# Performance work log

Hardware: AMD Instinct MI355X
Metric: run time of the kernel (lower is better)

## Reference

```python
import jax, jax.numpy as jnp
import numpy as np
import math

D_MODEL = 512
PATCH_LENS = (8, 16, 32)
MAX_P = 32
TAU = 0.5


def _sinusoid_pe(num_pos, d_model):
    pos = jnp.arange(num_pos, dtype=jnp.float32)[:, None]
    div = jnp.exp(jnp.arange(0, d_model, 2, dtype=jnp.float32) * (-(math.log(10000.0) / d_model)))
    pe = jnp.zeros((num_pos, d_model), dtype=jnp.float32)
    pe = pe.at[:, 0::2].set(jnp.sin(pos * div))
    pe = pe.at[:, 1::2].set(jnp.cos(pos * div))
    return pe  # [num_pos, d_model]


def setup_inputs() -> dict:
    key = jax.random.key(0)
    ks = jax.random.split(key, 10)
    B, C, L = 32, 64, 512
    BC, R, n_exp = B * C, L // MAX_P, len(PATCH_LENS)
    x = jax.random.normal(ks[0], (B, C, L), dtype=jnp.float32)
    u = jax.random.uniform(ks[1], (BC, R, n_exp), dtype=jnp.float32, minval=1e-6, maxval=1.0 - 1e-6)
    gumbel = -jnp.log(-jnp.log(u))
    # router MLP: Linear(max_patch_len, 64) -> ReLU -> Linear(64, n_exp)
    s1 = 1.0 / math.sqrt(MAX_P)
    s2 = 1.0 / math.sqrt(64)
    cls_w1 = jax.random.uniform(ks[2], (MAX_P, 64), jnp.float32, -s1, s1)
    cls_b1 = jax.random.uniform(ks[3], (64,), jnp.float32, -s1, s1)
    cls_w2 = jax.random.uniform(ks[4], (64, n_exp), jnp.float32, -s2, s2)
    cls_b2 = jax.random.uniform(ks[5], (n_exp,), jnp.float32, -s2, s2)
    # per-patch-length expert embeddings: Linear(p, d_model, bias=False)
    emb_w8 = jax.random.uniform(ks[6], (8, D_MODEL), jnp.float32, -1 / math.sqrt(8), 1 / math.sqrt(8))
    emb_w16 = jax.random.uniform(ks[7], (16, D_MODEL), jnp.float32, -1 / math.sqrt(16), 1 / math.sqrt(16))
    emb_w32 = jax.random.uniform(ks[8], (32, D_MODEL), jnp.float32, -1 / math.sqrt(32), 1 / math.sqrt(32))
    return {"x": x, "gumbel": gumbel, "cls_w1": cls_w1, "cls_b1": cls_b1,
            "cls_w2": cls_w2, "cls_b2": cls_b2,
            "emb_w8": emb_w8, "emb_w16": emb_w16, "emb_w32": emb_w32}


def reference(x, gumbel, cls_w1, cls_b1, cls_w2, cls_b2, emb_w8, emb_w16, emb_w32):
    B, C, L = x.shape
    R = L // MAX_P                    # regions per series
    T = MAX_P // min(PATCH_LENS)      # target patches per region (mode='fixed')
    n_exp = len(PATCH_LENS)
    xr = x.reshape(B * C, R, MAX_P)   # [BC, R, P]

    # router MLP per region (vectorized over all regions)
    h = jax.nn.relu(jnp.einsum('brp,pk->brk', xr, cls_w1) + cls_b1)
    logits = jnp.einsum('brk,kn->brn', h, cls_w2) + cls_b2   # [BC, R, n_exp]

    # gumbel-softmax (tau=0.5, hard=True, straight-through)
    y_soft = jax.nn.softmax((logits + gumbel) / TAU, axis=-1)
    idx = jnp.argmax(y_soft, axis=-1)                         # [BC, R]
    y_hard = jax.nn.one_hot(idx, n_exp, dtype=y_soft.dtype)
    cls_soft = y_hard - jax.lax.stop_gradient(y_soft) + y_soft
    cls_pred = jnp.argmax(cls_soft, axis=-1)                  # [BC, R]

    # multi-branch expert embeddings, aligned to T patches via repeat_interleave+truncate
    expert_ws = (emb_w8, emb_w16, emb_w32)
    embs = []
    for p, w in zip(PATCH_LENS, expert_ws):
        n_p = MAX_P // p
        patches = xr.reshape(B * C, R, n_p, p)               # unfold(-1, p, p)
        rep = T - n_p + 1                                     # repeat_interleave factor
        sel = jnp.arange(T) // rep                            # truncated interleave indices
        patches = patches[:, :, sel, :]                       # [BC, R, T, p]
        embs.append(jnp.einsum('brtp,pd->brtd', patches, w))  # [BC, R, T, d]
    stack = jnp.stack(embs, axis=0)                           # [n_exp, BC, R, T, d]

    gates = jnp.transpose(cls_soft, (2, 0, 1))[..., None, None]  # [n_exp, BC, R, 1, 1]
    region_emb = (stack * gates).sum(axis=0)                  # [BC, R, T, d]

    x_patch = region_emb.reshape(B * C, R * T, D_MODEL)
    x_patch = x_patch + _sinusoid_pe(R * T, D_MODEL)[None]

    all_cls_pred = cls_pred.T.reshape(-1)                     # cat over regions along dim 0
    return x_patch, all_cls_pred
```

## Files before the change

### kernel.cpp

```cpp
#include <hip/hip_runtime.h>
#include <hip/hip_bf16.h>

#define BC 2048
#define RR 16
#define DM 512
#define NREG (BC * RR)
#define XPATCH ((size_t)BC * 64 * DM)

__global__ __launch_bounds__(256) void ape_fused(
    const float* __restrict__ x,
    const float* __restrict__ gumbel,
    const float* __restrict__ w1,
    const float* __restrict__ b1,
    const float* __restrict__ w2,
    const float* __restrict__ b2,
    const float* __restrict__ w8,
    const float* __restrict__ w16,
    const float* __restrict__ w32,
    float* __restrict__ out)
{
    const int rid = blockIdx.x;
    const int bc  = rid >> 4;
    const int r   = rid & 15;
    const int tid = threadIdx.x;

    __shared__ float xs[32];
    __shared__ int sidx;

    if (tid < 32) xs[tid] = x[(size_t)bc * 512 + r * 32 + tid];
    __syncthreads();

    if (tid < 64) {
        float acc = b1[tid];
        #pragma unroll
        for (int q = 0; q < 32; ++q)
            acc = fmaf(xs[q], w1[q * 64 + tid], acc);
        float h = fmaxf(acc, 0.f);
        float p0 = h * w2[tid * 3 + 0];
        float p1 = h * w2[tid * 3 + 1];
        float p2 = h * w2[tid * 3 + 2];
        #pragma unroll
        for (int off = 32; off; off >>= 1) {
            p0 += __shfl_down(p0, off, 64);
            p1 += __shfl_down(p1, off, 64);
            p2 += __shfl_down(p2, off, 64);
        }
        if (tid == 0) {
            const float* g = gumbel + rid * 3;
            float s0 = p0 + b2[0] + g[0];
            float s1 = p1 + b2[1] + g[1];
            float s2 = p2 + b2[2] + g[2];
            int best = 0; float bs = s0;
            if (s1 > bs) { bs = s1; best = 1; }
            if (s2 > bs) { best = 2; }
            sidx = best;
            out[XPATCH + (size_t)r * BC + bc] = (float)best;
        }
    }
    __syncthreads();

    const int e  = sidx;
    const int d0 = tid * 2;

    auto dot = [&](const float* __restrict__ w, int xoff, int len) -> float2 {
        float2 acc = make_float2(0.f, 0.f);
        #pragma unroll
        for (int q = 0; q < len; ++q) {
            float2 wv = *reinterpret_cast<const float2*>(w + (size_t)q * DM + d0);
            float xv = xs[xoff + q];
            acc.x = fmaf(xv, wv.x, acc.x);
            acc.y = fmaf(xv, wv.y, acc.y);
        }
        return acc;
    };

    float2 a0, a1, a2, a3;
    if (e == 0) {
        a0 = dot(w8, 0, 8);
        a1 = dot(w8, 8, 8);
        a2 = dot(w8, 16, 8);
        a3 = dot(w8, 24, 8);
    } else if (e == 1) {
        a0 = dot(w16, 0, 16);
        a3 = dot(w16, 16, 16);
        a1 = a0; a2 = a0;
    } else {
        a0 = dot(w32, 0, 32);
        a1 = a0; a2 = a0; a3 = a0;
    }

    const float div = __expf((float)tid * (-9.210340371976184f / 256.0f));
    const int pos0 = r * 4;
    size_t obase = ((size_t)(bc * 64 + pos0)) * DM + d0;

    float2 av[4] = {a0, a1, a2, a3};
    #pragma unroll
    for (int t = 0; t < 4; ++t) {
        float sv, cv;
        __sincosf((float)(pos0 + t) * div, &sv, &cv);
        float2 o;
        o.x = av[t].x + sv;
        o.y = av[t].y + cv;
        *reinterpret_cast<float2*>(out + obase + (size_t)t * DM) = o;
    }
}

extern "C" void kernel_launch(void* const* d_in, const int* in_sizes, int n_in,
                              void* d_out, int out_size, void* d_ws, size_t ws_size,
                              hipStream_t stream) {
    const float* x      = (const float*)d_in[0];
    const float* gumbel = (const float*)d_in[1];
    const float* w1     = (const float*)d_in[2];
    const float* b1     = (const float*)d_in[3];
    const float* w2     = (const float*)d_in[4];
    const float* b2     = (const float*)d_in[5];
    const float* w8     = (const float*)d_in[6];
    const float* w16    = (const float*)d_in[7];
    const float* w32    = (const float*)d_in[8];
    float* out = (float*)d_out;

    ape_fused<<<NREG, 256, 0, stream>>>(x, gumbel, w1, b1, w2, b2, w8, w16, w32, out);
}
```

Baseline: 343.6 us.

## Process one series per block with bf16 expert weights staged in LDS

```diff
diff --git a/kernel.cpp b/kernel.cpp
--- a/kernel.cpp
+++ b/kernel.cpp
@@ -1,13 +1,29 @@
 #include <hip/hip_runtime.h>
 #include <hip/hip_bf16.h>
 
-#define BC 2048
-#define RR 16
 #define DM 512
-#define NREG (BC * RR)
-#define XPATCH ((size_t)BC * 64 * DM)
+#define BCN 2048
+#define NROW 56
+#define XPATCH ((size_t)BCN * 64 * DM)
 
-__global__ __launch_bounds__(256) void ape_fused(
+__device__ __forceinline__ unsigned pack_bf16(float a, float b) {
+    __hip_bfloat162 h = __float22bfloat162_rn(make_float2(a, b));
+    return *reinterpret_cast<unsigned*>(&h);
+}
+__device__ __forceinline__ float2 unpack_bf16(unsigned p) {
+    float2 r;
+    r.x = __uint_as_float(p << 16);
+    r.y = __uint_as_float(p & 0xffff0000u);
+    return r;
+}
+__device__ __forceinline__ void fma4(float4& a, float xv, float2 wa, float2 wb) {
+    a.x = fmaf(xv, wa.x, a.x);
+    a.y = fmaf(xv, wa.y, a.y);
+    a.z = fmaf(xv, wb.x, a.z);
+    a.w = fmaf(xv, wb.y, a.w);
+}
+
+__global__ __launch_bounds__(256, 2) void ape_fused(
     const float* __restrict__ x,
     const float* __restrict__ gumbel,
     const float* __restrict__ w1,
@@ -19,89 +35,139 @@
     const float* __restrict__ w32,
     float* __restrict__ out)
 {
-    const int rid = blockIdx.x;
-    const int bc  = rid >> 4;
-    const int r   = rid & 15;
+    __shared__ unsigned wlds[NROW * 256];
+    __shared__ float    xs[DM];
+    __shared__ int      eidx[16];
+
+    const int bc  = blockIdx.x;
     const int tid = threadIdx.x;
 
-    __shared__ float xs[32];
-    __shared__ int sidx;
+    if (tid < 128)
+        reinterpret_cast<float4*>(xs)[tid] =
+            reinterpret_cast<const float4*>(x + (size_t)bc * DM)[tid];
 
-    if (tid < 32) xs[tid] = x[(size_t)bc * 512 + r * 32 + tid];
+    #pragma unroll
+    for (int it = 0; it < 28; ++it) {
+        int f4   = it * 256 + tid;
+        int row  = f4 >> 7;
+        int col4 = f4 & 127;
+        const float* src = (row < 8)  ? (w8  + (size_t)row * DM)
+                         : (row < 24) ? (w16 + (size_t)(row - 8) * DM)
+                                      : (w32 + (size_t)(row - 24) * DM);
+        float4 v = reinterpret_cast<const float4*>(src)[col4];
+        uint2 pkd = make_uint2(pack_bf16(v.x, v.y), pack_bf16(v.z, v.w));
+        reinterpret_cast<uint2*>(wlds)[row * 128 + col4] = pkd;
+    }
     __syncthreads();
 
-    if (tid < 64) {
-        float acc = b1[tid];
+    {
+        const int lane = tid & 63;
+        const int wv   = tid >> 6;
+        float w1r[32];
         #pragma unroll
-        for (int q = 0; q < 32; ++q)
-            acc = fmaf(xs[q], w1[q * 64 + tid], acc);
-        float h = fmaxf(acc, 0.f);
-        float p0 = h * w2[tid * 3 + 0];
-        float p1 = h * w2[tid * 3 + 1];
-        float p2 = h * w2[tid * 3 + 2];
+        for (int q = 0; q < 32; ++q) w1r[q] = w1[q * 64 + lane];
+        const float w2r0 = w2[lane * 3 + 0];
+        const float w2r1 = w2[lane * 3 + 1];
+        const float w2r2 = w2[lane * 3 + 2];
+        const float b1r  = b1[lane];
+
+        float hh[4];
         #pragma unroll
-        for (int off = 32; off; off >>= 1) {
-            p0 += __shfl_down(p0, off, 64);
-            p1 += __shfl_down(p1, off, 64);
-            p2 += __shfl_down(p2, off, 64);
+        for (int p = 0; p < 4; ++p) {
+            const int rr = p * 4 + wv;
+            const float* xr = xs + rr * 32;
+            float a = b1r;
+            #pragma unroll
+            for (int q = 0; q < 32; ++q) a = fmaf(xr[q], w1r[q], a);
+            hh[p] = fmaxf(a, 0.f);
         }
-        if (tid == 0) {
-            const float* g = gumbel + rid * 3;
-            float s0 = p0 + b2[0] + g[0];
-            float s1 = p1 + b2[1] + g[1];
-            float s2 = p2 + b2[2] + g[2];
-            int best = 0; float bs = s0;
-            if (s1 > bs) { bs = s1; best = 1; }
-            if (s2 > bs) { best = 2; }
-            sidx = best;
-            out[XPATCH + (size_t)r * BC + bc] = (float)best;
+        #pragma unroll
+        for (int p = 0; p < 4; ++p) {
+            float p0 = hh[p] * w2r0, p1 = hh[p] * w2r1, p2 = hh[p] * w2r2;
+            #pragma unroll
+            for (int off = 32; off; off >>= 1) {
+                p0 += __shfl_down(p0, off, 64);
+                p1 += __shfl_down(p1, off, 64);
+                p2 += __shfl_down(p2, off, 64);
+            }
+            if (lane == 0) {
+                const int rr = p * 4 + wv;
+                const float* g = gumbel + ((size_t)bc * 16 + rr) * 3;
+                float s0 = p0 + b2[0] + g[0];
+                float s1 = p1 + b2[1] + g[1];
+                float s2 = p2 + b2[2] + g[2];
+                int best = 0; float bs = s0;
+                if (s1 > bs) { bs = s1; best = 1; }
+                if (s2 > bs) { best = 2; }
+                eidx[rr] = best;
+                out[XPATCH + (size_t)rr * BCN + bc] = (float)best;
+            }
         }
     }
     __syncthreads();
 
-    const int e  = sidx;
-    const int d0 = tid * 2;
+    const int rp = tid >> 7;
+    const int cg = tid & 127;
+    const int c0 = cg * 4;
+    const float kln = -9.210340371976184f / 256.0f;
+    const float dv0 = __expf((float)(cg * 2)     * kln);
+    const float dv1 = __expf((float)(cg * 2 + 1) * kln);
+    const uint2* wbase = reinterpret_cast<const uint2*>(wlds) + cg;
 
-    auto dot = [&](const float* __restrict__ w, int xoff, int len) -> float2 {
-        float2 acc = make_float2(0.f, 0.f);
+    #pragma unroll 1
+    for (int p = 0; p < 8; ++p) {
+        const int rr = p * 2 + rp;
+        const int e  = eidx[rr];
+        const int xo = rr * 32;
+        float4 a0 = {0,0,0,0}, a1 = {0,0,0,0}, a2 = {0,0,0,0}, a3 = {0,0,0,0};
+
+        if (e == 0) {
+            const uint2* wp = wbase;
+            #pragma unroll
+            for (int q = 0; q < 8; ++q) {
+                uint2 pk = wp[q * 128];
+                float2 wa = unpack_bf16(pk.x), wb = unpack_bf16(pk.y);
+                fma4(a0, xs[xo + q],      wa, wb);
+                fma4(a1, xs[xo + 8  + q], wa, wb);
+                fma4(a2, xs[xo + 16 + q], wa, wb);
+                fma4(a3, xs[xo + 24 + q], wa, wb);
+            }
+        } else if (e == 1) {
+            const uint2* wp = wbase + 8 * 128;
+            #pragma unroll
+            for (int q = 0; q < 16; ++q) {
+                uint2 pk = wp[q * 128];
+                float2 wa = unpack_bf16(pk.x), wb = unpack_bf16(pk.y);
+                fma4(a0, xs[xo + q],      wa, wb);
+                fma4(a3, xs[xo + 16 + q], wa, wb);
+            }
+            a1 = a0; a2 = a0;
+        } else {
+            const uint2* wp = wbase + 24 * 128;
+            #pragma unroll
+            for (int q = 0; q < 32; ++q) {
+                uint2 pk = wp[q * 128];
+                float2 wa = unpack_bf16(pk.x), wb = unpack_bf16(pk.y);
+                fma4(a0, xs[xo + q], wa, wb);
+            }
+            a1 = a0; a2 = a0; a3 = a0;
+        }
+
+        const size_t ob = ((size_t)(bc * 64 + rr * 4)) * DM + c0;
+        float4 av[4] = {a0, a1, a2, a3};
         #pragma unroll
-        for (int q = 0; q < len; ++q) {
-            float2 wv = *reinterpret_cast<const float2*>(w + (size_t)q * DM + d0);
-            float xv = xs[xoff + q];
-            acc.x = fmaf(xv, wv.x, acc.x);
-            acc.y = fmaf(xv, wv.y, acc.y);
+        for (int t = 0; t < 4; ++t) {
+            float sv0, cv0, sv1, cv1;
+            const float pos = (float)(rr * 4 + t);
+            __sincosf(pos * dv0, &sv0, &cv0);
+            __sincosf(pos * dv1, &sv1, &cv1);
+            float4 o;
+            o.x = av[t].x + sv0;
+            o.y = av[t].y + cv0;
+            o.z = av[t].z + sv1;
+            o.w = av[t].w + cv1;
+            *reinterpret_cast<float4*>(out + ob + (size_t)t * DM) = o;
         }
-        return acc;
-    };
-
-    float2 a0, a1, a2, a3;
-    if (e == 0) {
-        a0 = dot(w8, 0, 8);
-        a1 = dot(w8, 8, 8);
-        a2 = dot(w8, 16, 8);
-        a3 = dot(w8, 24, 8);
-    } else if (e == 1) {
-        a0 = dot(w16, 0, 16);
-        a3 = dot(w16, 16, 16);
-        a1 = a0; a2 = a0;
-    } else {
-        a0 = dot(w32, 0, 32);
-        a1 = a0; a2 = a0; a3 = a0;
-    }
-
-    const float div = __expf((float)tid * (-9.210340371976184f / 256.0f));
-    const int pos0 = r * 4;
-    size_t obase = ((size_t)(bc * 64 + pos0)) * DM + d0;
-
-    float2 av[4] = {a0, a1, a2, a3};
-    #pragma unroll
-    for (int t = 0; t < 4; ++t) {
-        float sv, cv;
-        __sincosf((float)(pos0 + t) * div, &sv, &cv);
-        float2 o;
-        o.x = av[t].x + sv;
-        o.y = av[t].y + cv;
-        *reinterpret_cast<float2*>(out + obase + (size_t)t * DM) = o;
     }
 }
 
@@ -119,5 +185,5 @@
     const float* w32    = (const float*)d_in[8];
     float* out = (float*)d_out;
 
-    ape_fused<<<NREG, 256, 0, stream>>>(x, gumbel, w1, b1, w2, b2, w8, w16, w32, out);
+    ape_fused<<<BCN, 256, 0, stream>>>(x, gumbel, w1, b1, w2, b2, w8, w16, w32, out);
 }
```

After: 302.1 us. 12.1% less time.
